# Kernel tuning notes

Measured on AMD Instinct MI355X. Metric: run time of the kernel, lower is better.

## Reference

```python
import jax, jax.numpy as jnp
import numpy as np

NL, D, H, DH, DFF, DIN, MAXLEN = 3, 128, 4, 32, 512, 64, 4096
B, L = 2, 2048


def setup_inputs() -> dict:
    key = jax.random.key(0)
    ks = jax.random.split(key, 10)
    def n(k, shape, s=0.02):
        return jax.random.normal(k, shape, jnp.float32) * s
    return dict(
        x=jax.random.normal(ks[0], (B, L, DIN), jnp.float32),
        embed_w=n(ks[1], (D, DIN)), embed_b=jnp.zeros((D,), jnp.float32),
        pos_emb=n(ks[2], (MAXLEN + 1, D)),
        cls=n(ks[3], (1, 1, D)),
        in_proj_w=n(ks[4], (NL, 3 * D, D)), in_proj_b=jnp.zeros((NL, 3 * D), jnp.float32),
        out_w=n(ks[5], (NL, D, D)), out_b=jnp.zeros((NL, D), jnp.float32),
        ln1_s=jnp.ones((NL, D), jnp.float32), ln1_b=jnp.zeros((NL, D), jnp.float32),
        ln2_s=jnp.ones((NL, D), jnp.float32), ln2_b=jnp.zeros((NL, D), jnp.float32),
        ff1_w=n(ks[6], (NL, DFF, D)), ff1_b=jnp.zeros((NL, DFF), jnp.float32),
        ff2_w=n(ks[7], (NL, D, DFF)), ff2_b=jnp.zeros((NL, D), jnp.float32),
        head_ln_s=jnp.ones((D,), jnp.float32), head_ln_b=jnp.zeros((D,), jnp.float32),
        head_w=n(ks[8], (1, D)), head_b=jnp.zeros((1,), jnp.float32),
    )


def _ln(x, s, b, eps=1e-5):
    m = x.mean(-1, keepdims=True)
    v = ((x - m) ** 2).mean(-1, keepdims=True)
    return (x - m) * jax.lax.rsqrt(v + eps) * s + b


def reference(x, embed_w, embed_b, pos_emb, cls, in_proj_w, in_proj_b, out_w, out_b,
              ln1_s, ln1_b, ln2_s, ln2_b, ff1_w, ff1_b, ff2_w, ff2_b,
              head_ln_s, head_ln_b, head_w, head_b):
    b, l, _ = x.shape
    # token embedding + positional embeddings at indices 1..L (0 reserved for CLS)
    h = x @ embed_w.T + embed_b + pos_emb[1:l + 1]            # [B,L,D]
    cls_tok = jnp.broadcast_to(cls + pos_emb[0], (b, 1, D))   # CLS gets pos_emb[0]
    h = jnp.concatenate([cls_tok, h], axis=1)                 # [B,S,D], S=L+1
    s = l + 1
    scale = 1.0 / np.sqrt(DH).astype(np.float32)
    for i in range(NL):  # norm_first encoder layers, eager MHA (dropout=0 / eval)
        hn = _ln(h, ln1_s[i], ln1_b[i])
        qkv = hn @ in_proj_w[i].T + in_proj_b[i]
        q, k, v = jnp.split(qkv, 3, axis=-1)
        q = q.reshape(b, s, H, DH)
        k = k.reshape(b, s, H, DH)
        v = v.reshape(b, s, H, DH)
        attn = jax.nn.softmax(jnp.einsum('bqhd,bkhd->bhqk', q, k) * scale, axis=-1)
        o = jnp.einsum('bhqk,bkhd->bqhd', attn, v).reshape(b, s, D)
        h = h + o @ out_w[i].T + out_b[i]
        hn = _ln(h, ln2_s[i], ln2_b[i])
        h = h + jax.nn.relu(hn @ ff1_w[i].T + ff1_b[i]) @ ff2_w[i].T + ff2_b[i]
    pooled = _ln(h[:, 0], head_ln_s, head_ln_b)               # CLS pooling
    return (pooled @ head_w.T + head_b)[:, 0]                 # [B]
```

## Files before the change

kernel.cpp:

```cpp
#include <hip/hip_runtime.h>

typedef unsigned short u16;
typedef float f32x4 __attribute__((ext_vector_type(4)));
typedef short short8 __attribute__((ext_vector_type(8)));

#define S_LEN 2049
#define SP    2112
#define BS    4098
#define MROWS 4112
#define KSPLIT 8

__device__ __forceinline__ float b2f(u16 u){
  unsigned int i = ((unsigned int)u) << 16; float f; __builtin_memcpy(&f, &i, 4); return f;
}
__device__ __forceinline__ u16 f2b(float f){
  unsigned int i; __builtin_memcpy(&i, &f, 4);
  unsigned int r = i + 0x7FFFu + ((i >> 16) & 1u);
  return (u16)(r >> 16);
}

enum {
  OFF_X = 0,            OFF_EW = 262144,  OFF_EB = 270336,  OFF_POS = 270464,
  OFF_CLS = 794880,     OFF_IPW = 795008, OFF_IPB = 942464, OFF_OW = 943616,
  OFF_OB = 992768,      OFF_L1S = 993152, OFF_L1B = 993536, OFF_L2S = 993920,
  OFF_L2B = 994304,     OFF_F1W = 994688, OFF_F1B = 1191296, OFF_F2W = 1192832,
  OFF_F2B = 1389440,    OFF_HLS = 1389824, OFF_HLB = 1389952, OFF_HW = 1390080,
  OFF_HB = 1390208,     OFF_END = 1390209, CANON_PAD = 1390216
};

struct CArgs { const void* s[21]; };

__global__ __launch_bounds__(256) void convert_kernel(CArgs a, u16* __restrict__ dst){
  const int offs[22] = {OFF_X,OFF_EW,OFF_EB,OFF_POS,OFF_CLS,OFF_IPW,OFF_IPB,OFF_OW,OFF_OB,
    OFF_L1S,OFF_L1B,OFF_L2S,OFF_L2B,OFF_F1W,OFF_F1B,OFF_F2W,OFF_F2B,OFF_HLS,OFF_HLB,
    OFF_HW,OFF_HB,OFF_END};
  int tid = blockIdx.x * 256 + threadIdx.x;
  if (tid >= OFF_END) return;
  int lo = 0, hi = 21;
  while (hi - lo > 1){ int mid = (lo + hi) >> 1; if (tid >= offs[mid]) lo = mid; else hi = mid; }
  int local = tid - offs[lo];
  dst[tid] = f2b(((const float*)a.s[lo])[local]);
}

__global__ void zero_pad_kernel(u16* __restrict__ qkv){
  int i = blockIdx.x * 256 + threadIdx.x;
  if (i >= 24 * 63 * 32) return;
  int wb = i / 2016;
  int r  = i - wb * 2016;
  int s  = S_LEN + r / 32;
  int dh = r & 31;
  qkv[((size_t)wb * SP + s) * 32 + dh] = 0;
}

__global__ __launch_bounds__(128) void embed_kernel(const u16* __restrict__ cw, float* __restrict__ h)
{
  __shared__ float xs[64];
  int t = blockIdx.x;
  int b = (t >= S_LEN) ? 1 : 0;
  int s = t - b * S_LEN;
  int d = threadIdx.x;
  float val;
  if (s == 0){
    val = b2f(cw[OFF_CLS + d]) + b2f(cw[OFF_POS + d]);
  } else {
    const u16* xr = cw + OFF_X + ((size_t)b * 2048 + (s - 1)) * 64;
    if (d < 64) xs[d] = b2f(xr[d]);
    __syncthreads();
    const u16* wr = cw + OFF_EW + (size_t)d * 64;
    float acc = 0.f;
#pragma unroll
    for (int j = 0; j < 64; j += 4){
      ushort4 wv = *(const ushort4*)(wr + j);
      acc += b2f(wv.x) * xs[j] + b2f(wv.y) * xs[j+1] + b2f(wv.z) * xs[j+2] + b2f(wv.w) * xs[j+3];
    }
    val = acc + b2f(cw[OFF_EB + d]) + b2f(cw[OFF_POS + (size_t)s * 128 + d]);
  }
  h[(size_t)t * 128 + d] = val;
}

__global__ __launch_bounds__(256) void ln_kernel(
    const float* __restrict__ h, const u16* __restrict__ g, const u16* __restrict__ be,
    u16* __restrict__ hn)
{
  int lane = threadIdx.x & 63;
  int t = blockIdx.x * 4 + (threadIdx.x >> 6);
  if (t >= BS) return;
  const float* row = h + (size_t)t * 128;
  float e0 = row[lane], e1 = row[lane + 64];
  float sm = e0 + e1;
  sm += __shfl_xor(sm,1,64); sm += __shfl_xor(sm,2,64); sm += __shfl_xor(sm,4,64);
  sm += __shfl_xor(sm,8,64); sm += __shfl_xor(sm,16,64); sm += __shfl_xor(sm,32,64);
  float mean = sm * (1.f/128.f);
  float d0 = e0 - mean, d1 = e1 - mean;
  float vv = d0*d0 + d1*d1;
  vv += __shfl_xor(vv,1,64); vv += __shfl_xor(vv,2,64); vv += __shfl_xor(vv,4,64);
  vv += __shfl_xor(vv,8,64); vv += __shfl_xor(vv,16,64); vv += __shfl_xor(vv,32,64);
  float rstd = rsqrtf(vv * (1.f/128.f) + 1e-5f);
  u16* o = hn + (size_t)t * 128;
  o[lane]      = f2b(d0 * rstd * b2f(g[lane])      + b2f(be[lane]));
  o[lane + 64] = f2b(d1 * rstd * b2f(g[lane + 64]) + b2f(be[lane + 64]));
}

template<int K, int N, int MODE>
__global__ __launch_bounds__(256) void gemm_kernel(
    const u16* __restrict__ A, const u16* __restrict__ W, const u16* __restrict__ bias,
    float* __restrict__ hres, u16* __restrict__ out)
{
  constexpr int NT  = N / 16;
  constexpr int TOT = 257 * NT;
  int lane = threadIdx.x & 63;
  int wave = blockIdx.x * 4 + (threadIdx.x >> 6);
  if (wave >= TOT) return;
  int mt = wave / NT, nt = wave - mt * NT;
  int mi = lane & 15, quad = lane >> 4;
  const u16* Ap = A + (size_t)(mt * 16 + mi) * K + quad * 8;
  const u16* Wp = W + (size_t)(nt * 16 + mi) * K + quad * 8;
  f32x4 acc = {0.f, 0.f, 0.f, 0.f};
#pragma unroll
  for (int kc = 0; kc < K / 32; kc++){
    short8 a = *(const short8*)(Ap + kc * 32);
    short8 b = *(const short8*)(Wp + kc * 32);
    acc = __builtin_amdgcn_mfma_f32_16x16x32_bf16(a, b, acc, 0, 0, 0);
  }
  int n = nt * 16 + mi;
  float bv = b2f(bias[n]);
#pragma unroll
  for (int r = 0; r < 4; r++){
    int m = mt * 16 + quad * 4 + r;
    if (m >= BS) continue;
    float v = acc[r] + bv;
    if (MODE == 0){
      int which = n >> 7, d = n & 127, hd = d >> 5, dh = d & 31;
      int b_ = (m >= S_LEN) ? 1 : 0;
      int s  = m - b_ * S_LEN;
      out[(size_t)(((which * 2 + b_) * 4 + hd) * SP + s) * 32 + dh] = f2b(v);
    } else if (MODE == 1){
      hres[(size_t)m * 128 + n] += v;
    } else {
      out[(size_t)m * N + n] = f2b(v > 0.f ? v : 0.f);
    }
  }
}

__global__ __launch_bounds__(256, 8) void attn_kernel(
    const u16* __restrict__ qkv, float* __restrict__ Opart, float* __restrict__ Lpart)
{
  __shared__ u16 Kl[64 * 40];
  __shared__ u16 Vt[32 * 72];
  __shared__ u16 Pl[4][16 * 72];
  int tid = threadIdx.x;
  int lane = tid & 63, w = tid >> 6;
  int qt = blockIdx.x, bh = blockIdx.y, split = blockIdx.z;
  const u16* Qb = qkv + (size_t)bh * SP * 32;
  const u16* Kb = qkv + (size_t)(8 + bh) * SP * 32;
  const u16* Vb = qkv + (size_t)(16 + bh) * SP * 32;
  int mi = lane & 15, quad = lane >> 4;
  int q0 = qt * 64 + w * 16;
  short8 qf = *(const short8*)(Qb + (size_t)(q0 + mi) * 32 + quad * 8);
  f32x4 o0 = {0,0,0,0}, o1 = {0,0,0,0};
  float lp[4] = {0.f, 0.f, 0.f, 0.f};
  int c0 = (split * 33) >> 3, c1 = ((split + 1) * 33) >> 3;
  int kkey = tid >> 2, kdh = (tid & 3) * 8;
  int vdh = tid & 31, vgrp = tid >> 5;
  u16* Pw = Pl[w];
  for (int c = c0; c < c1; c++){
    int kb = c * 64;
    __syncthreads();
    *(short8*)&Kl[kkey * 40 + kdh] = *(const short8*)(Kb + (size_t)(kb + kkey) * 32 + kdh);
    {
      const u16* vb = Vb + (size_t)(kb + vgrp * 4) * 32 + vdh;
      ushort4 a, b;
      a.x = vb[0];    a.y = vb[32];   a.z = vb[64];   a.w = vb[96];
      b.x = vb[1024]; b.y = vb[1056]; b.z = vb[1088]; b.w = vb[1120];
      *(ushort4*)&Vt[vdh * 72 + vgrp * 4] = a;
      *(ushort4*)&Vt[vdh * 72 + (vgrp + 8) * 4] = b;
    }
    __syncthreads();
#pragma unroll
    for (int kt = 0; kt < 4; kt++){
      short8 kf = *(const short8*)&Kl[(kt * 16 + mi) * 40 + quad * 8];
      f32x4 z = {0,0,0,0};
      f32x4 s = __builtin_amdgcn_mfma_f32_16x16x32_bf16(qf, kf, z, 0, 0, 0);
      bool val = (kb + kt * 16 + mi) < S_LEN;
#pragma unroll
      for (int r = 0; r < 4; r++){
        float aa = fminf(fmaxf(s[r] * 0.25503486f, -30.f), 30.f);
        float p = val ? exp2f(aa) : 0.f;
        lp[r] += p;
        Pw[(quad * 4 + r) * 72 + kt * 16 + mi] = f2b(p);
      }
    }
    short8 pf0 = *(const short8*)&Pw[mi * 72 + quad * 8];
    short8 pf1 = *(const short8*)&Pw[mi * 72 + 32 + quad * 8];
    short8 va0 = *(const short8*)&Vt[mi * 72 + quad * 8];
    short8 va1 = *(const short8*)&Vt[mi * 72 + 32 + quad * 8];
    short8 vb0 = *(const short8*)&Vt[(16 + mi) * 72 + quad * 8];
    short8 vb1 = *(const short8*)&Vt[(16 + mi) * 72 + 32 + quad * 8];
    o0 = __builtin_amdgcn_mfma_f32_16x16x32_bf16(pf0, va0, o0, 0, 0, 0);
    o0 = __builtin_amdgcn_mfma_f32_16x16x32_bf16(pf1, va1, o0, 0, 0, 0);
    o1 = __builtin_amdgcn_mfma_f32_16x16x32_bf16(pf0, vb0, o1, 0, 0, 0);
    o1 = __builtin_amdgcn_mfma_f32_16x16x32_bf16(pf1, vb1, o1, 0, 0, 0);
  }
#pragma unroll
  for (int r = 0; r < 4; r++){
    lp[r] += __shfl_xor(lp[r], 1, 64); lp[r] += __shfl_xor(lp[r], 2, 64);
    lp[r] += __shfl_xor(lp[r], 4, 64); lp[r] += __shfl_xor(lp[r], 8, 64);
  }
  size_t pb = ((size_t)qt * 8 + bh) * KSPLIT + split;
  float* Ob = Opart + pb * 2048 + (size_t)w * 16 * 32;
#pragma unroll
  for (int r = 0; r < 4; r++){
    Ob[(quad * 4 + r) * 32 + mi]      = o0[r];
    Ob[(quad * 4 + r) * 32 + 16 + mi] = o1[r];
  }
  if (mi == 0){
#pragma unroll
    for (int r = 0; r < 4; r++)
      Lpart[pb * 64 + w * 16 + quad * 4 + r] = lp[r];
  }
}

__global__ __launch_bounds__(256) void attn_reduce_kernel(
    const float* __restrict__ Opart, const float* __restrict__ Lpart, u16* __restrict__ aout)
{
  __shared__ float linv[64];
  int qt = blockIdx.x, bh = blockIdx.y;
  int tid = threadIdx.x;
  size_t pb0 = ((size_t)qt * 8 + bh) * KSPLIT;
  if (tid < 64){
    float ls = 0.f;
#pragma unroll
    for (int s = 0; s < KSPLIT; s++) ls += Lpart[(pb0 + s) * 64 + tid];
    linv[tid] = 1.f / fmaxf(ls, 1e-30f);
  }
  __syncthreads();
  int e = tid * 8;
  f32x4 s0 = {0,0,0,0}, s1 = {0,0,0,0};
#pragma unroll
  for (int s = 0; s < KSPLIT; s++){
    const float* base = Opart + (pb0 + s) * 2048 + e;
    s0 += *(const f32x4*)base;
    s1 += *(const f32x4*)(base + 4);
  }
  int q = e >> 5;
  int tok = qt * 64 + q;
  if (tok < S_LEN){
    int bq = bh >> 2, hh = bh & 3;
    float inv = linv[q];
    ushort4 w0, w1;
    w0.x = f2b(s0[0]*inv); w0.y = f2b(s0[1]*inv); w0.z = f2b(s0[2]*inv); w0.w = f2b(s0[3]*inv);
    w1.x = f2b(s1[0]*inv); w1.y = f2b(s1[1]*inv); w1.z = f2b(s1[2]*inv); w1.w = f2b(s1[3]*inv);
    u16* dst = aout + ((size_t)bq * S_LEN + tok) * 128 + hh * 32 + (e & 31);
    *(ushort4*)dst = w0;
    *(ushort4*)(dst + 4) = w1;
  }
}

__global__ __launch_bounds__(128) void head_kernel(
    const float* __restrict__ h, const u16* __restrict__ cw, float* __restrict__ out)
{
  __shared__ float red[128];
  int tid = threadIdx.x;
  for (int b = 0; b < 2; b++){
    float e = h[(size_t)b * S_LEN * 128 + tid];
    red[tid] = e; __syncthreads();
    for (int st = 64; st > 0; st >>= 1){ if (tid < st) red[tid] += red[tid + st]; __syncthreads(); }
    float mean = red[0] * (1.f/128.f); __syncthreads();
    float d = e - mean; red[tid] = d * d; __syncthreads();
    for (int st = 64; st > 0; st >>= 1){ if (tid < st) red[tid] += red[tid + st]; __syncthreads(); }
    float rstd = rsqrtf(red[0] * (1.f/128.f) + 1e-5f); __syncthreads();
    float val = d * rstd * b2f(cw[OFF_HLS + tid]) + b2f(cw[OFF_HLB + tid]);
    red[tid] = val * b2f(cw[OFF_HW + tid]); __syncthreads();
    for (int st = 64; st > 0; st >>= 1){ if (tid < st) red[tid] += red[tid + st]; __syncthreads(); }
    if (tid == 0) out[b] = red[0] + b2f(cw[OFF_HB]);
    __syncthreads();
  }
}

extern "C" void kernel_launch(void* const* d_in, const int* in_sizes, int n_in,
                              void* d_out, int out_size, void* d_ws, size_t ws_size,
                              hipStream_t stream)
{
  char* ws = (char*)d_ws;
  u16* cw     = (u16*)ws;    ws += (size_t)CANON_PAD * 2;
  float* h    = (float*)ws;  ws += (size_t)MROWS * 128 * 4;
  u16* hn     = (u16*)ws;    ws += (size_t)MROWS * 128 * 2;
  u16* qkv    = (u16*)ws;    ws += (size_t)24 * SP * 32 * 2;
  u16* aout   = (u16*)ws;    ws += (size_t)MROWS * 128 * 2;
  u16* f1     = (u16*)ws;    ws += (size_t)MROWS * 512 * 2;
  float* Opart= (float*)ws;  ws += (size_t)33 * 8 * KSPLIT * 2048 * 4;
  float* Lpart= (float*)ws;  ws += (size_t)33 * 8 * KSPLIT * 64 * 4;

  CArgs ca;
  for (int i = 0; i < 21; i++) ca.s[i] = d_in[i];

  convert_kernel<<<dim3((OFF_END + 255) / 256), dim3(256), 0, stream>>>(ca, cw);
  zero_pad_kernel<<<dim3((24 * 63 * 32 + 255) / 256), dim3(256), 0, stream>>>(qkv);
  embed_kernel<<<dim3(BS), dim3(128), 0, stream>>>(cw, h);
  for (int l = 0; l < 3; l++){
    ln_kernel<<<dim3((BS + 3) / 4), dim3(256), 0, stream>>>(
        h, cw + OFF_L1S + l * 128, cw + OFF_L1B + l * 128, hn);
    gemm_kernel<128, 384, 0><<<dim3(1542), dim3(256), 0, stream>>>(
        hn, cw + OFF_IPW + (size_t)l * 384 * 128, cw + OFF_IPB + l * 384, nullptr, qkv);
    attn_kernel<<<dim3(33, 8, KSPLIT), dim3(256), 0, stream>>>(qkv, Opart, Lpart);
    attn_reduce_kernel<<<dim3(33, 8), dim3(256), 0, stream>>>(Opart, Lpart, aout);
    gemm_kernel<128, 128, 1><<<dim3(514), dim3(256), 0, stream>>>(
        aout, cw + OFF_OW + (size_t)l * 128 * 128, cw + OFF_OB + l * 128, h, nullptr);
    ln_kernel<<<dim3((BS + 3) / 4), dim3(256), 0, stream>>>(
        h, cw + OFF_L2S + l * 128, cw + OFF_L2B + l * 128, hn);
    gemm_kernel<128, 512, 2><<<dim3(2056), dim3(256), 0, stream>>>(
        hn, cw + OFF_F1W + (size_t)l * 512 * 128, cw + OFF_F1B + l * 512, nullptr, f1);
    gemm_kernel<512, 128, 1><<<dim3(514), dim3(256), 0, stream>>>(
        f1, cw + OFF_F2W + (size_t)l * 128 * 512, cw + OFF_F2B + l * 128, h, nullptr);
  }
  head_kernel<<<dim3(1), dim3(128), 0, stream>>>(h, cw, (float*)d_out);
}
```

Before: 335.6 us.

## Fuse LayerNorm into GEMM prologues, MFMA embedding, merge init kernels

Removes the standalone LayerNorm kernels and the hn buffer: each QKV and FF1 GEMM wave now loads fp32 rows of h, computes mean and variance with cross-quad shuffles, and builds normalized bf16 A fragments in registers. The embedding is rewritten as an MFMA GEMM, and the convert, zero-pad and CLS-token initialization are merged into a single init kernel. Together these cut kernel launches and the write and re-read of the normalized activations. In exchange each N-tile wave recomputes LN for its 16 rows, which is redundant work, and the attention kernel's exp clamp is removed and its occupancy bound lowered.

```diff
diff --git a/kernel.cpp b/kernel.cpp
--- a/kernel.cpp
+++ b/kernel.cpp
@@ -30,81 +30,60 @@
 
 struct CArgs { const void* s[21]; };
 
-__global__ __launch_bounds__(256) void convert_kernel(CArgs a, u16* __restrict__ dst){
+__global__ __launch_bounds__(256) void init_kernel(
+    CArgs a, u16* __restrict__ dst, u16* __restrict__ qkv, float* __restrict__ h)
+{
   const int offs[22] = {OFF_X,OFF_EW,OFF_EB,OFF_POS,OFF_CLS,OFF_IPW,OFF_IPB,OFF_OW,OFF_OB,
     OFF_L1S,OFF_L1B,OFF_L2S,OFF_L2B,OFF_F1W,OFF_F1B,OFF_F2W,OFF_F2B,OFF_HLS,OFF_HLB,
     OFF_HW,OFF_HB,OFF_END};
   int tid = blockIdx.x * 256 + threadIdx.x;
+  if (tid < 24 * 63 * 32){
+    int wb = tid / 2016;
+    int r  = tid - wb * 2016;
+    qkv[((size_t)wb * SP + S_LEN + r / 32) * 32 + (r & 31)] = 0;
+  }
+  if (tid < 256){
+    int d = tid & 127, b = tid >> 7;
+    h[(size_t)b * S_LEN * 128 + d] =
+        ((const float*)a.s[4])[d] + ((const float*)a.s[3])[d];
+  }
   if (tid >= OFF_END) return;
   int lo = 0, hi = 21;
   while (hi - lo > 1){ int mid = (lo + hi) >> 1; if (tid >= offs[mid]) lo = mid; else hi = mid; }
-  int local = tid - offs[lo];
-  dst[tid] = f2b(((const float*)a.s[lo])[local]);
-}
-
-__global__ void zero_pad_kernel(u16* __restrict__ qkv){
-  int i = blockIdx.x * 256 + threadIdx.x;
-  if (i >= 24 * 63 * 32) return;
-  int wb = i / 2016;
-  int r  = i - wb * 2016;
-  int s  = S_LEN + r / 32;
-  int dh = r & 31;
-  qkv[((size_t)wb * SP + s) * 32 + dh] = 0;
-}
-
-__global__ __launch_bounds__(128) void embed_kernel(const u16* __restrict__ cw, float* __restrict__ h)
-{
-  __shared__ float xs[64];
-  int t = blockIdx.x;
-  int b = (t >= S_LEN) ? 1 : 0;
-  int s = t - b * S_LEN;
-  int d = threadIdx.x;
-  float val;
-  if (s == 0){
-    val = b2f(cw[OFF_CLS + d]) + b2f(cw[OFF_POS + d]);
-  } else {
-    const u16* xr = cw + OFF_X + ((size_t)b * 2048 + (s - 1)) * 64;
-    if (d < 64) xs[d] = b2f(xr[d]);
-    __syncthreads();
-    const u16* wr = cw + OFF_EW + (size_t)d * 64;
-    float acc = 0.f;
-#pragma unroll
-    for (int j = 0; j < 64; j += 4){
-      ushort4 wv = *(const ushort4*)(wr + j);
-      acc += b2f(wv.x) * xs[j] + b2f(wv.y) * xs[j+1] + b2f(wv.z) * xs[j+2] + b2f(wv.w) * xs[j+3];
-    }
-    val = acc + b2f(cw[OFF_EB + d]) + b2f(cw[OFF_POS + (size_t)s * 128 + d]);
-  }
-  h[(size_t)t * 128 + d] = val;
-}
-
-__global__ __launch_bounds__(256) void ln_kernel(
-    const float* __restrict__ h, const u16* __restrict__ g, const u16* __restrict__ be,
-    u16* __restrict__ hn)
+  dst[tid] = f2b(((const float*)a.s[lo])[tid - offs[lo]]);
+}
+
+__global__ __launch_bounds__(256) void embed_kernel(const u16* __restrict__ cw, float* __restrict__ h)
 {
   int lane = threadIdx.x & 63;
-  int t = blockIdx.x * 4 + (threadIdx.x >> 6);
-  if (t >= BS) return;
-  const float* row = h + (size_t)t * 128;
-  float e0 = row[lane], e1 = row[lane + 64];
-  float sm = e0 + e1;
-  sm += __shfl_xor(sm,1,64); sm += __shfl_xor(sm,2,64); sm += __shfl_xor(sm,4,64);
-  sm += __shfl_xor(sm,8,64); sm += __shfl_xor(sm,16,64); sm += __shfl_xor(sm,32,64);
-  float mean = sm * (1.f/128.f);
-  float d0 = e0 - mean, d1 = e1 - mean;
-  float vv = d0*d0 + d1*d1;
-  vv += __shfl_xor(vv,1,64); vv += __shfl_xor(vv,2,64); vv += __shfl_xor(vv,4,64);
-  vv += __shfl_xor(vv,8,64); vv += __shfl_xor(vv,16,64); vv += __shfl_xor(vv,32,64);
-  float rstd = rsqrtf(vv * (1.f/128.f) + 1e-5f);
-  u16* o = hn + (size_t)t * 128;
-  o[lane]      = f2b(d0 * rstd * b2f(g[lane])      + b2f(be[lane]));
-  o[lane + 64] = f2b(d1 * rstd * b2f(g[lane + 64]) + b2f(be[lane + 64]));
-}
-
-template<int K, int N, int MODE>
-__global__ __launch_bounds__(256) void gemm_kernel(
-    const u16* __restrict__ A, const u16* __restrict__ W, const u16* __restrict__ bias,
-    float* __restrict__ hres, u16* __restrict__ out)
+  int wave = blockIdx.x * 4 + (threadIdx.x >> 6);
+  int mt = wave >> 3, nt = wave & 7;
+  int mi = lane & 15, quad = lane >> 4;
+  const u16* Ap = cw + OFF_X + (size_t)(mt * 16 + mi) * 64 + quad * 8;
+  const u16* Wp = cw + OFF_EW + (size_t)(nt * 16 + mi) * 64 + quad * 8;
+  f32x4 acc = {0.f, 0.f, 0.f, 0.f};
+#pragma unroll
+  for (int kc = 0; kc < 2; kc++){
+    short8 av = *(const short8*)(Ap + kc * 32);
+    short8 wv = *(const short8*)(Wp + kc * 32);
+    acc = __builtin_amdgcn_mfma_f32_16x16x32_bf16(av, wv, acc, 0, 0, 0);
+  }
+  int n = nt * 16 + mi;
+  float ebv = b2f(cw[OFF_EB + n]);
+#pragma unroll
+  for (int r = 0; r < 4; r++){
+    int m = mt * 16 + quad * 4 + r;
+    int b = m >> 11, s = (m & 2047) + 1;
+    h[((size_t)b * S_LEN + s) * 128 + n] =
+        acc[r] + ebv + b2f(cw[OFF_POS + (size_t)s * 128 + n]);
+  }
+}
+
+template<int N, int MODE>
+__global__ __launch_bounds__(256, 4) void lngemm_kernel(
+    const u16* __restrict__ cw, const float* __restrict__ h,
+    const u16* __restrict__ g, const u16* __restrict__ be,
+    const u16* __restrict__ W, const u16* __restrict__ bias, u16* __restrict__ out)
 {
   constexpr int NT  = N / 16;
   constexpr int TOT = 257 * NT;
@@ -113,6 +92,69 @@
   if (wave >= TOT) return;
   int mt = wave / NT, nt = wave - mt * NT;
   int mi = lane & 15, quad = lane >> 4;
+  const float* hrow = h + (size_t)(mt * 16 + mi) * 128 + quad * 8;
+  float v[32];
+  float sm = 0.f;
+#pragma unroll
+  for (int kc = 0; kc < 4; kc++){
+    f32x4 x0 = *(const f32x4*)(hrow + kc * 32);
+    f32x4 x1 = *(const f32x4*)(hrow + kc * 32 + 4);
+#pragma unroll
+    for (int j = 0; j < 4; j++){ v[kc*8+j] = x0[j]; v[kc*8+4+j] = x1[j]; }
+    sm += x0[0]+x0[1]+x0[2]+x0[3]+x1[0]+x1[1]+x1[2]+x1[3];
+  }
+  sm += __shfl_xor(sm, 16, 64); sm += __shfl_xor(sm, 32, 64);
+  float mean = sm * (1.f/128.f);
+  float vv = 0.f;
+#pragma unroll
+  for (int j = 0; j < 32; j++){ float d = v[j] - mean; vv += d * d; }
+  vv += __shfl_xor(vv, 16, 64); vv += __shfl_xor(vv, 32, 64);
+  float rstd = rsqrtf(vv * (1.f/128.f) + 1e-5f);
+  short8 af[4];
+#pragma unroll
+  for (int kc = 0; kc < 4; kc++){
+    short8 gs = *(const short8*)(g  + kc * 32 + quad * 8);
+    short8 bs = *(const short8*)(be + kc * 32 + quad * 8);
+#pragma unroll
+    for (int j = 0; j < 8; j++)
+      af[kc][j] = (short)f2b((v[kc*8+j] - mean) * rstd * b2f((u16)gs[j]) + b2f((u16)bs[j]));
+  }
+  const u16* Wp = W + (size_t)(nt * 16 + mi) * 128 + quad * 8;
+  f32x4 acc = {0.f, 0.f, 0.f, 0.f};
+#pragma unroll
+  for (int kc = 0; kc < 4; kc++){
+    short8 wv = *(const short8*)(Wp + kc * 32);
+    acc = __builtin_amdgcn_mfma_f32_16x16x32_bf16(af[kc], wv, acc, 0, 0, 0);
+  }
+  int n = nt * 16 + mi;
+  float bv = b2f(bias[n]);
+#pragma unroll
+  for (int r = 0; r < 4; r++){
+    int m = mt * 16 + quad * 4 + r;
+    if (m >= BS) continue;
+    float val = acc[r] + bv;
+    if (MODE == 0){
+      int which = n >> 7, d = n & 127, hd = d >> 5, dh = d & 31;
+      int b_ = (m >= S_LEN) ? 1 : 0;
+      int s  = m - b_ * S_LEN;
+      out[(size_t)(((which * 2 + b_) * 4 + hd) * SP + s) * 32 + dh] = f2b(val);
+    } else {
+      out[(size_t)m * N + n] = f2b(val > 0.f ? val : 0.f);
+    }
+  }
+}
+
+template<int K>
+__global__ __launch_bounds__(256) void gemm_res_kernel(
+    const u16* __restrict__ A, const u16* __restrict__ W, const u16* __restrict__ bias,
+    float* __restrict__ hres)
+{
+  constexpr int TOT = 257 * 8;
+  int lane = threadIdx.x & 63;
+  int wave = blockIdx.x * 4 + (threadIdx.x >> 6);
+  if (wave >= TOT) return;
+  int mt = wave >> 3, nt = wave & 7;
+  int mi = lane & 15, quad = lane >> 4;
   const u16* Ap = A + (size_t)(mt * 16 + mi) * K + quad * 8;
   const u16* Wp = W + (size_t)(nt * 16 + mi) * K + quad * 8;
   f32x4 acc = {0.f, 0.f, 0.f, 0.f};
@@ -128,21 +170,11 @@
   for (int r = 0; r < 4; r++){
     int m = mt * 16 + quad * 4 + r;
     if (m >= BS) continue;
-    float v = acc[r] + bv;
-    if (MODE == 0){
-      int which = n >> 7, d = n & 127, hd = d >> 5, dh = d & 31;
-      int b_ = (m >= S_LEN) ? 1 : 0;
-      int s  = m - b_ * S_LEN;
-      out[(size_t)(((which * 2 + b_) * 4 + hd) * SP + s) * 32 + dh] = f2b(v);
-    } else if (MODE == 1){
-      hres[(size_t)m * 128 + n] += v;
-    } else {
-      out[(size_t)m * N + n] = f2b(v > 0.f ? v : 0.f);
-    }
-  }
-}
-
-__global__ __launch_bounds__(256, 8) void attn_kernel(
+    hres[(size_t)m * 128 + n] += acc[r] + bv;
+  }
+}
+
+__global__ __launch_bounds__(256, 4) void attn_kernel(
     const u16* __restrict__ qkv, float* __restrict__ Opart, float* __restrict__ Lpart)
 {
   __shared__ u16 Kl[64 * 40];
@@ -184,8 +216,7 @@
       bool val = (kb + kt * 16 + mi) < S_LEN;
 #pragma unroll
       for (int r = 0; r < 4; r++){
-        float aa = fminf(fmaxf(s[r] * 0.25503486f, -30.f), 30.f);
-        float p = val ? exp2f(aa) : 0.f;
+        float p = val ? exp2f(s[r] * 0.25503486f) : 0.f;
         lp[r] += p;
         Pw[(quad * 4 + r) * 72 + kt * 16 + mi] = f2b(p);
       }
@@ -284,7 +315,6 @@
   char* ws = (char*)d_ws;
   u16* cw     = (u16*)ws;    ws += (size_t)CANON_PAD * 2;
   float* h    = (float*)ws;  ws += (size_t)MROWS * 128 * 4;
-  u16* hn     = (u16*)ws;    ws += (size_t)MROWS * 128 * 2;
   u16* qkv    = (u16*)ws;    ws += (size_t)24 * SP * 32 * 2;
   u16* aout   = (u16*)ws;    ws += (size_t)MROWS * 128 * 2;
   u16* f1     = (u16*)ws;    ws += (size_t)MROWS * 512 * 2;
@@ -294,24 +324,21 @@
   CArgs ca;
   for (int i = 0; i < 21; i++) ca.s[i] = d_in[i];
 
-  convert_kernel<<<dim3((OFF_END + 255) / 256), dim3(256), 0, stream>>>(ca, cw);
-  zero_pad_kernel<<<dim3((24 * 63 * 32 + 255) / 256), dim3(256), 0, stream>>>(qkv);
-  embed_kernel<<<dim3(BS), dim3(128), 0, stream>>>(cw, h);
+  init_kernel<<<dim3((OFF_END + 255) / 256), dim3(256), 0, stream>>>(ca, cw, qkv, h);
+  embed_kernel<<<dim3(512), dim3(256), 0, stream>>>(cw, h);
   for (int l = 0; l < 3; l++){
-    ln_kernel<<<dim3((BS + 3) / 4), dim3(256), 0, stream>>>(
-        h, cw + OFF_L1S + l * 128, cw + OFF_L1B + l * 128, hn);
-    gemm_kernel<128, 384, 0><<<dim3(1542), dim3(256), 0, stream>>>(
-        hn, cw + OFF_IPW + (size_t)l * 384 * 128, cw + OFF_IPB + l * 384, nullptr, qkv);
+    lngemm_kernel<384, 0><<<dim3(1542), dim3(256), 0, stream>>>(
+        cw, h, cw + OFF_L1S + l * 128, cw + OFF_L1B + l * 128,
+        cw + OFF_IPW + (size_t)l * 384 * 128, cw + OFF_IPB + l * 384, qkv);
     attn_kernel<<<dim3(33, 8, KSPLIT), dim3(256), 0, stream>>>(qkv, Opart, Lpart);
     attn_reduce_kernel<<<dim3(33, 8), dim3(256), 0, stream>>>(Opart, Lpart, aout);
-    gemm_kernel<128, 128, 1><<<dim3(514), dim3(256), 0, stream>>>(
-        aout, cw + OFF_OW + (size_t)l * 128 * 128, cw + OFF_OB + l * 128, h, nullptr);
-    ln_kernel<<<dim3((BS + 3) / 4), dim3(256), 0, stream>>>(
-        h, cw + OFF_L2S + l * 128, cw + OFF_L2B + l * 128, hn);
-    gemm_kernel<128, 512, 2><<<dim3(2056), dim3(256), 0, stream>>>(
-        hn, cw + OFF_F1W + (size_t)l * 512 * 128, cw + OFF_F1B + l * 512, nullptr, f1);
-    gemm_kernel<512, 128, 1><<<dim3(514), dim3(256), 0, stream>>>(
-        f1, cw + OFF_F2W + (size_t)l * 128 * 512, cw + OFF_F2B + l * 128, h, nullptr);
+    gemm_res_kernel<128><<<dim3(514), dim3(256), 0, stream>>>(
+        aout, cw + OFF_OW + (size_t)l * 128 * 128, cw + OFF_OB + l * 128, h);
+    lngemm_kernel<512, 2><<<dim3(2056), dim3(256), 0, stream>>>(
+        cw, h, cw + OFF_L2S + l * 128, cw + OFF_L2B + l * 128,
+        cw + OFF_F1W + (size_t)l * 512 * 128, cw + OFF_F1B + l * 512, f1);
+    gemm_res_kernel<512><<<dim3(514), dim3(256), 0, stream>>>(
+        f1, cw + OFF_F2W + (size_t)l * 128 * 512, cw + OFF_F2B + l * 128, h);
   }
   head_kernel<<<dim3(1), dim3(128), 0, stream>>>(h, cw, (float*)d_out);
 }
```

Result: no change. 335.2 us (-0.1%).
